# Optimization experiments

Measured on AMD Instinct MI355X. Metric: run time of the kernel, lower is better.

Reference implementation:

```python
import jax, jax.numpy as jnp
import numpy as np

L, H, E, T, B, V = 8, 16, 1024, 1024, 2, 800
D = E // H  # head_size = 64
STD = 0.02


def setup_inputs() -> dict:
    key = jax.random.key(0)
    ks = iter(jax.random.split(key, 32))

    def nrm(shape):
        return jax.random.normal(next(ks), shape, jnp.float32) * STD

    latlong = jax.random.uniform(next(ks), (B, T, 2), jnp.float32)
    wl = jax.random.uniform(next(ks), (B, T, 1), jnp.float32, minval=3.0, maxval=11.0)
    inp = {
        "idx": jnp.concatenate([latlong, wl], axis=-1),  # [B,T,3]
        "tok_table": nrm((V, E)),
        "pos_W": nrm((2, E)),
        "pos_b": jnp.zeros((E,), jnp.float32),
        # stacked per-layer params (per-head q/k/v linears fused into [E,E])
        "Wq": nrm((L, E, E)),
        "Wk": nrm((L, E, E)),
        "Wv": nrm((L, E, E)),
        "Wo": nrm((L, E, E)),
        "bo": jnp.zeros((L, E), jnp.float32),
        "W1": nrm((L, E, 4 * E)),
        "b1": jnp.zeros((L, 4 * E), jnp.float32),
        "W2": nrm((L, 4 * E, E)),
        "b2": jnp.zeros((L, E), jnp.float32),
        "ln1_g": jnp.ones((L, E), jnp.float32),
        "ln1_b": jnp.zeros((L, E), jnp.float32),
        "ln2_g": jnp.ones((L, E), jnp.float32),
        "ln2_b": jnp.zeros((L, E), jnp.float32),
        "lnf_g": jnp.ones((E,), jnp.float32),
        "lnf_b": jnp.zeros((E,), jnp.float32),
        "lm_W": nrm((E, V)),
        "lm_b": jnp.zeros((V,), jnp.float32),
    }
    return inp


def _ln(x, g, b, eps=1e-5):
    m = x.mean(-1, keepdims=True)
    v = x.var(-1, keepdims=True)
    return (x - m) * jax.lax.rsqrt(v + eps) * g + b


def _block(x, p):
    Wq, Wk, Wv, Wo, bo, W1, b1, W2, b2, g1, be1, g2, be2 = p
    Bx, Tx, _ = x.shape
    h = _ln(x, g1, be1)
    q = (h @ Wq).reshape(Bx, Tx, H, D)
    k = (h @ Wk).reshape(Bx, Tx, H, D)
    v = (h @ Wv).reshape(Bx, Tx, H, D)
    scores = jnp.einsum('bqhd,bkhd->bhqk', q, k) * (D ** -0.5)
    mask = jnp.tril(jnp.ones((Tx, Tx), bool))  # causal
    scores = jnp.where(mask, scores, -jnp.inf)
    w = jax.nn.softmax(scores, axis=-1)  # dropout=0 (eval) -> identity
    attn = jnp.einsum('bhqk,bkhd->bqhd', w, v).reshape(Bx, Tx, E)
    x = x + attn @ Wo + bo
    h = _ln(x, g2, be2)
    x = x + jax.nn.relu(h @ W1 + b1) @ W2 + b2
    return x


def reference(idx, tok_table, pos_W, pos_b, Wq, Wk, Wv, Wo, bo, W1, b1, W2, b2,
              ln1_g, ln1_b, ln2_g, ln2_b, lnf_g, lnf_b, lm_W, lm_b):
    # water level channel -> token id in [0, V-1]
    idx_wl = jnp.clip(jnp.round(idx[..., 2] * 100.0 - 300.0), 0, V - 1).astype(jnp.int32)
    tok_emb = tok_table[idx_wl]                      # [B,T,E]
    pos_emb = idx[..., :2] @ pos_W + pos_b           # [B,T,E]
    x = tok_emb + pos_emb

    params = (Wq, Wk, Wv, Wo, bo, W1, b1, W2, b2, ln1_g, ln1_b, ln2_g, ln2_b)

    def body(carry, p):
        return _block(carry, p), None

    x, _ = jax.lax.scan(body, x, params)
    x = _ln(x, lnf_g, lnf_b)
    logits = x @ lm_W + lm_b                         # [B,T,V]
    return logits
```

## Files before the change

kernel.cpp:

```cpp
#include <hip/hip_runtime.h>
#include <hip/hip_bf16.h>

#define L_ 8
#define H_ 16
#define E_ 1024
#define T_ 1024
#define B_ 2
#define V_ 800
#define D_ 64
#define FF_ 4096
#define N_ (B_ * T_)
#define QS_ 3072

typedef unsigned short u16;
typedef __bf16 bf16x8 __attribute__((ext_vector_type(8)));
typedef float f32x4 __attribute__((ext_vector_type(4)));

__device__ __forceinline__ u16 f2b(float f) {
    unsigned int u = __float_as_uint(f);
    unsigned int r = (u + 0x7fffu + ((u >> 16) & 1u)) >> 16;
    return (u16)r;
}

__device__ __forceinline__ void gld16(const u16* g, u16* l) {
    __builtin_amdgcn_global_load_lds(
        (__attribute__((address_space(1))) void*)(uintptr_t)g,
        (__attribute__((address_space(3))) void*)(unsigned)(uintptr_t)l,
        16, 0, 0);
}

__global__ __launch_bounds__(256) void embed_k(
    const float* __restrict__ idx, const float* __restrict__ tok,
    const float* __restrict__ posW, const float* __restrict__ posb,
    float* __restrict__ x)
{
    int row = blockIdx.x;
    int e = threadIdx.x * 4;
    float lat = idx[row * 3 + 0];
    float lon = idx[row * 3 + 1];
    float wl  = idx[row * 3 + 2];
    float tf = rintf(wl * 100.0f - 300.0f);
    tf = fminf(fmaxf(tf, 0.0f), (float)(V_ - 1));
    int tkn = (int)tf;

    float4 tv = *(const float4*)(tok + (size_t)tkn * E_ + e);
    float4 p0 = *(const float4*)(posW + e);
    float4 p1 = *(const float4*)(posW + E_ + e);
    float4 pb = *(const float4*)(posb + e);
    float4 ov;
    ov.x = tv.x + lat * p0.x + lon * p1.x + pb.x;
    ov.y = tv.y + lat * p0.y + lon * p1.y + pb.y;
    ov.z = tv.z + lat * p0.z + lon * p1.z + pb.z;
    ov.w = tv.w + lat * p0.w + lon * p1.w + pb.w;
    *(float4*)(x + (size_t)row * E_ + e) = ov;
}

__global__ __launch_bounds__(256) void ln_k(
    const float* __restrict__ x, const float* __restrict__ g,
    const float* __restrict__ bta, u16* __restrict__ out)
{
    __shared__ float rs[4], rq[4];
    int row = blockIdx.x;
    int tid = threadIdx.x;
    const float* xr = x + (size_t)row * E_;
    float4 xv = *(const float4*)(xr + tid * 4);
    float s = xv.x + xv.y + xv.z + xv.w;
    float q = xv.x * xv.x + xv.y * xv.y + xv.z * xv.z + xv.w * xv.w;
    #pragma unroll
    for (int off = 32; off; off >>= 1) {
        s += __shfl_xor(s, off, 64);
        q += __shfl_xor(q, off, 64);
    }
    int wv = tid >> 6, ln = tid & 63;
    if (ln == 0) { rs[wv] = s; rq[wv] = q; }
    __syncthreads();
    s = rs[0] + rs[1] + rs[2] + rs[3];
    q = rq[0] + rq[1] + rq[2] + rq[3];
    float mean = s * (1.0f / E_);
    float var  = q * (1.0f / E_) - mean * mean;
    float inv  = 1.0f / sqrtf(var + 1e-5f);
    int c = tid * 4;
    float4 gv = *(const float4*)(g + c);
    float4 bv = *(const float4*)(bta + c);
    ushort4 ov;
    ov.x = f2b((xv.x - mean) * inv * gv.x + bv.x);
    ov.y = f2b((xv.y - mean) * inv * gv.y + bv.y);
    ov.z = f2b((xv.z - mean) * inv * gv.z + bv.z);
    ov.w = f2b((xv.w - mean) * inv * gv.w + bv.w);
    *(ushort4*)(out + (size_t)row * E_ + c) = ov;
}

__global__ __launch_bounds__(256) void comb_ln_k(
    const float* __restrict__ Cp, const float* __restrict__ bias,
    float* __restrict__ x, const float* __restrict__ g,
    const float* __restrict__ bta, u16* __restrict__ hout)
{
    __shared__ float rs[4], rq[4];
    int row = blockIdx.x;
    int tid = threadIdx.x;
    int c = tid * 4;
    size_t off = (size_t)row * E_ + c;
    const size_t total = (size_t)N_ * E_;
    float4 p0 = *(const float4*)(Cp + off);
    float4 p1 = *(const float4*)(Cp + total + off);
    float4 xv = *(const float4*)(x + off);
    float4 bv = *(const float4*)(bias + c);
    xv.x += p0.x + p1.x + bv.x;
    xv.y += p0.y + p1.y + bv.y;
    xv.z += p0.z + p1.z + bv.z;
    xv.w += p0.w + p1.w + bv.w;
    *(float4*)(x + off) = xv;

    float s = xv.x + xv.y + xv.z + xv.w;
    float q = xv.x * xv.x + xv.y * xv.y + xv.z * xv.z + xv.w * xv.w;
    #pragma unroll
    for (int o = 32; o; o >>= 1) {
        s += __shfl_xor(s, o, 64);
        q += __shfl_xor(q, o, 64);
    }
    int wv = tid >> 6, ln = tid & 63;
    if (ln == 0) { rs[wv] = s; rq[wv] = q; }
    __syncthreads();
    s = rs[0] + rs[1] + rs[2] + rs[3];
    q = rq[0] + rq[1] + rq[2] + rq[3];
    float mean = s * (1.0f / E_);
    float var  = q * (1.0f / E_) - mean * mean;
    float inv  = 1.0f / sqrtf(var + 1e-5f);
    float4 gv = *(const float4*)(g + c);
    float4 bb = *(const float4*)(bta + c);
    ushort4 ov;
    ov.x = f2b((xv.x - mean) * inv * gv.x + bb.x);
    ov.y = f2b((xv.y - mean) * inv * gv.y + bb.y);
    ov.z = f2b((xv.z - mean) * inv * gv.z + bb.z);
    ov.w = f2b((xv.w - mean) * inv * gv.w + bb.w);
    *(ushort4*)(hout + off) = ov;
}

__device__ __forceinline__ void wtrans_body(
    const float* __restrict__ W, u16* __restrict__ Wt, int K, int M,
    int m0, int k0)
{
    __shared__ float tile[64][65];
    int tid = threadIdx.x;
    int rr = tid >> 4, c4 = (tid & 15) * 4;
    if (m0 + 64 <= M) {
        #pragma unroll
        for (int p = 0; p < 4; p++) {
            int kk = rr + p * 16;
            float4 v4 = *(const float4*)(W + (size_t)(k0 + kk) * M + m0 + c4);
            tile[kk][c4 + 0] = v4.x; tile[kk][c4 + 1] = v4.y;
            tile[kk][c4 + 2] = v4.z; tile[kk][c4 + 3] = v4.w;
        }
    } else {
        #pragma unroll
        for (int p = 0; p < 4; p++) {
            int kk = rr + p * 16;
            const float* wr = W + (size_t)(k0 + kk) * M;
            #pragma unroll
            for (int c = 0; c < 4; c++) {
                int m = m0 + c4 + c;
                tile[kk][c4 + c] = (m < M) ? wr[m] : 0.0f;
            }
        }
    }
    __syncthreads();
    #pragma unroll
    for (int p = 0; p < 4; p++) {
        int ml = rr + p * 16;
        ushort4 o;
        o.x = f2b(tile[c4 + 0][ml]);
        o.y = f2b(tile[c4 + 1][ml]);
        o.z = f2b(tile[c4 + 2][ml]);
        o.w = f2b(tile[c4 + 3][ml]);
        *(ushort4*)(Wt + (size_t)(m0 + ml) * K + k0 + c4) = o;
    }
}

__global__ __launch_bounds__(256) void wtrans_k(
    const float* __restrict__ W, u16* __restrict__ Wt, int K, int M)
{
    wtrans_body(W, Wt, K, M, blockIdx.x * 64, blockIdx.y * 64);
}

__global__ __launch_bounds__(256) void wtrans_all_k(
    const float* __restrict__ Wq, const float* __restrict__ Wk,
    const float* __restrict__ Wv, const float* __restrict__ Wo,
    const float* __restrict__ W1, const float* __restrict__ W2,
    u16* __restrict__ wqkv_t, u16* __restrict__ wo_t,
    u16* __restrict__ w1_t, u16* __restrict__ w2_t)
{
    int bx = blockIdx.x, by = blockIdx.y, z = blockIdx.z;
    const size_t M1 = 1024 * 1024;
    if (z < 4) {
        if (bx >= 16) return;
        const float* W = (z == 0) ? Wq : (z == 1) ? Wk : (z == 2) ? Wv : Wo;
        u16* dst = (z < 3) ? (wqkv_t + (size_t)z * M1) : wo_t;
        wtrans_body(W, dst, E_, E_, bx * 64, by * 64);
    } else if (z == 4) {
        wtrans_body(W1, w1_t, E_, FF_, bx * 64, by * 64);
    } else {
        int id = by * 64 + bx;
        int mb = id >> 6, kb = id & 63;
        wtrans_body(W2, w2_t, FF_, E_, mb * 64, kb * 64);
    }
}

__global__ __launch_bounds__(256) void gemm_bf16(
    const u16* __restrict__ A, const u16* __restrict__ Bt,
    const float* __restrict__ bias, const float* __restrict__ res,
    float* __restrict__ Cf, u16* __restrict__ Cb, float* __restrict__ Cp,
    int K, int M, int relu)
{
    __shared__ __align__(16) u16 As[128 * 32];
    __shared__ __align__(16) u16 Bs[128 * 32];
    int tid = threadIdx.x;
    int bm = blockIdx.y * 128, bn = blockIdx.x * 128;
    int zz = blockIdx.z;
    int kslice = K / (int)gridDim.z;
    int lane = tid & 63, wv = tid >> 6;
    int l15 = lane & 15, q4 = lane >> 4;
    int wm = (wv & 1) * 64, wn = (wv >> 1) * 64;

    const u16* ga = A + (size_t)(bm + (tid >> 2)) * K + zz * kslice + (tid & 3) * 8;
    const u16* gb = Bt + (size_t)(bn + (tid >> 2)) * K + zz * kslice + (tid & 3) * 8;
    size_t gstep = (size_t)64 * K;
    u16* lA0 = As + wv * (16 * 32);
    u16* lB0 = Bs + wv * (16 * 32);

    f32x4 acc[4][4];
    #pragma unroll
    for (int i = 0; i < 4; i++)
        #pragma unroll
        for (int j = 0; j < 4; j++)
            acc[i][j] = (f32x4){0.0f, 0.0f, 0.0f, 0.0f};

    for (int k0 = 0; k0 < kslice; k0 += 32) {
        gld16(ga, lA0);
        gld16(ga + gstep, lA0 + 64 * 32);
        gld16(gb, lB0);
        gld16(gb + gstep, lB0 + 64 * 32);
        ga += 32; gb += 32;
        __syncthreads();

        const bf16x8* Ap = (const bf16x8*)As + (wm + l15) * 4 + q4;
        const bf16x8* Bp = (const bf16x8*)Bs + (wn + l15) * 4 + q4;
        bf16x8 af[4], bg[4];
        #pragma unroll
        for (int i = 0; i < 4; i++) { af[i] = Ap[i * 64]; bg[i] = Bp[i * 64]; }
        #pragma unroll
        for (int i = 0; i < 4; i++)
            #pragma unroll
            for (int j = 0; j < 4; j++)
                acc[i][j] = __builtin_amdgcn_mfma_f32_16x16x32_bf16(
                    af[i], bg[j], acc[i][j], 0, 0, 0);
        __syncthreads();
    }

    size_t poff = (size_t)zz * N_ * M;
    #pragma unroll
    for (int i = 0; i < 4; i++) {
        int r0 = bm + wm + i * 16 + q4 * 4;
        #pragma unroll
        for (int j = 0; j < 4; j++) {
            int col = bn + wn + j * 16 + l15;
            if (col < M) {
                if (Cp) {
                    #pragma unroll
                    for (int r = 0; r < 4; r++)
                        Cp[poff + (size_t)(r0 + r) * M + col] = acc[i][j][r];
                } else {
                    float bv = bias ? bias[col] : 0.0f;
                    #pragma unroll
                    for (int r = 0; r < 4; r++) {
                        size_t off = (size_t)(r0 + r) * M + col;
                        float v = acc[i][j][r] + bv;
                        if (res) v += res[off];
                        if (relu) v = fmaxf(v, 0.0f);
                        if (Cb) Cb[off] = f2b(v); else Cf[off] = v;
                    }
                }
            }
        }
    }
}

__global__ __launch_bounds__(256) void combine_k(
    const float* __restrict__ Cp, const float* __restrict__ bias,
    float* __restrict__ Cf, int M, int total)
{
    int e = (blockIdx.x * 256 + threadIdx.x) * 4;
    if (e >= total) return;
    float4 a = *(const float4*)(Cp + e);
    float4 b = *(const float4*)(Cp + (size_t)total + e);
    a.x += b.x; a.y += b.y; a.z += b.z; a.w += b.w;
    int col = e % M;
    if (bias) {
        float4 bv = *(const float4*)(bias + col);
        a.x += bv.x; a.y += bv.y; a.z += bv.z; a.w += bv.w;
    }
    *(float4*)(Cf + e) = a;
}

__global__ __launch_bounds__(256) void vtrans_k(
    const u16* __restrict__ QKV, u16* __restrict__ Vt)
{
    __shared__ u16 tile[64][72];
    int t0 = blockIdx.x * 64, h = blockIdx.y, b = blockIdx.z;
    int tid = threadIdx.x;
    int row = tid >> 3, c8 = (tid & 7) * 8;
    #pragma unroll
    for (int p = 0; p < 2; p++) {
        int t = row + p * 32;
        *(float4*)&tile[t][c8] = *(const float4*)(
            QKV + (size_t)(b * T_ + t0 + t) * QS_ + 2 * E_ + h * D_ + c8);
    }
    __syncthreads();
    #pragma unroll
    for (int p = 0; p < 2; p++) {
        int d = row + p * 32;
        u16 o[8];
        #pragma unroll
        for (int j = 0; j < 8; j++) o[j] = tile[c8 + j][d];
        *(ushort4*)(Vt + ((size_t)(b * H_ + h) * D_ + d) * T_ + t0 + c8) =
            *(ushort4*)&o[0];
        *(ushort4*)(Vt + ((size_t)(b * H_ + h) * D_ + d) * T_ + t0 + c8 + 4) =
            *(ushort4*)&o[4];
    }
}

__global__ __launch_bounds__(256) void attn_mfma_k(
    const u16* __restrict__ QKV, const u16* __restrict__ Vt,
    u16* __restrict__ O)
{
    __shared__ __align__(16) u16 Ps[4][16 * 72];
    int tid = threadIdx.x;
    int wv = tid >> 6, lane = tid & 63;
    int c = lane & 15, q4 = lane >> 4;
    int qb = (int)(gridDim.x - 1) - (int)blockIdx.x;
    int h = blockIdx.y, b = blockIdx.z;
    int q0 = qb * 64 + wv * 16;
    const float scale = 0.125f;

    const u16* qrow = QKV + (size_t)(b * T_ + q0 + c) * QS_ + h * D_;
    bf16x8 qf0 = *(const bf16x8*)(qrow + q4 * 8);
    bf16x8 qf1 = *(const bf16x8*)(qrow + 32 + q4 * 8);

    const u16* kbase  = QKV + (size_t)b * T_ * QS_ + E_ + h * D_;
    const u16* vtbase = Vt + (size_t)(b * H_ + h) * D_ * T_;

    float l_acc[4] = {0.0f, 0.0f, 0.0f, 0.0f};
    f32x4 acc_o[4];
    #pragma unroll
    for (int nt = 0; nt < 4; nt++) acc_o[nt] = (f32x4){0.f, 0.f, 0.f, 0.f};

    u16* ps = &Ps[wv][0];

    for (int kt = 0; kt <= qb; kt++) {
        int k0 = kt * 64;
        bool diag = (kt == qb);

        bf16x8 kf[4][2];
        #pragma unroll
        for (int j = 0; j < 4; j++) {
            const u16* kr = kbase + (size_t)(k0 + 16 * j + c) * QS_ + q4 * 8;
            kf[j][0] = *(const bf16x8*)(kr);
            kf[j][1] = *(const bf16x8*)(kr + 32);
        }

        #pragma unroll
        for (int j = 0; j < 4; j++) {
            f32x4 sa = (f32x4){0.f, 0.f, 0.f, 0.f};
            sa = __builtin_amdgcn_mfma_f32_16x16x32_bf16(qf0, kf[j][0], sa, 0, 0, 0);
            sa = __builtin_amdgcn_mfma_f32_16x16x32_bf16(qf1, kf[j][1], sa, 0, 0, 0);
            #pragma unroll
            for (int r = 0; r < 4; r++) {
                bool masked = diag && (k0 + 16 * j + c > q0 + 4 * q4 + r);
                float pj = masked ? 0.0f : __expf(sa[r] * scale);
                l_acc[r] += pj;
                ps[(4 * q4 + r) * 72 + 16 * j + c] = f2b(pj);
            }
        }
        bf16x8 pf0 = *(const bf16x8*)(ps + c * 72 + q4 * 8);
        bf16x8 pf1 = *(const bf16x8*)(ps + c * 72 + 32 + q4 * 8);

        bf16x8 vf[4][2];
        #pragma unroll
        for (int nt = 0; nt < 4; nt++) {
            const u16* vr = vtbase + (size_t)(16 * nt + c) * T_ + k0 + q4 * 8;
            vf[nt][0] = *(const bf16x8*)(vr);
            vf[nt][1] = *(const bf16x8*)(vr + 32);
        }

        #pragma unroll
        for (int nt = 0; nt < 4; nt++) {
            acc_o[nt] = __builtin_amdgcn_mfma_f32_16x16x32_bf16(pf0, vf[nt][0], acc_o[nt], 0, 0, 0);
            acc_o[nt] = __builtin_amdgcn_mfma_f32_16x16x32_bf16(pf1, vf[nt][1], acc_o[nt], 0, 0, 0);
        }
    }

    #pragma unroll
    for (int r = 0; r < 4; r++) {
        float ts = l_acc[r];
        ts += __shfl_xor(ts, 1, 64);
        ts += __shfl_xor(ts, 2, 64);
        ts += __shfl_xor(ts, 4, 64);
        ts += __shfl_xor(ts, 8, 64);
        l_acc[r] = ts;
    }

    #pragma unroll
    for (int r = 0; r < 4; r++) {
        float inv = 1.0f / l_acc[r];
        size_t orow = (size_t)(b * T_ + q0 + 4 * q4 + r) * E_ + h * D_;
        #pragma unroll
        for (int nt = 0; nt < 4; nt++)
            O[orow + 16 * nt + c] = f2b(acc_o[nt][r] * inv);
    }
}

extern "C" void kernel_launch(void* const* d_in, const int* in_sizes, int n_in,
                              void* d_out, int out_size, void* d_ws, size_t ws_size,
                              hipStream_t stream)
{
    const float* idx   = (const float*)d_in[0];
    const float* tok   = (const float*)d_in[1];
    const float* posW  = (const float*)d_in[2];
    const float* posb  = (const float*)d_in[3];
    const float* Wq    = (const float*)d_in[4];
    const float* Wk    = (const float*)d_in[5];
    const float* Wv    = (const float*)d_in[6];
    const float* Wo    = (const float*)d_in[7];
    const float* bo    = (const float*)d_in[8];
    const float* W1    = (const float*)d_in[9];
    const float* b1    = (const float*)d_in[10];
    const float* W2    = (const float*)d_in[11];
    const float* b2    = (const float*)d_in[12];
    const float* ln1g  = (const float*)d_in[13];
    const float* ln1b  = (const float*)d_in[14];
    const float* ln2g  = (const float*)d_in[15];
    const float* ln2b  = (const float*)d_in[16];
    const float* lnfg  = (const float*)d_in[17];
    const float* lnfb  = (const float*)d_in[18];
    const float* lmW   = (const float*)d_in[19];
    const float* lmb   = (const float*)d_in[20];
    float* out = (float*)d_out;

    const size_t M1 = 1024 * 1024;
    float* ws    = (float*)d_ws;
    float* x     = ws;
    float* cpart = x + 2 * M1;
    u16* qkv   = (u16*)(cpart + 4 * M1);
    u16* vt    = qkv + 6 * M1;
    u16* h_bf  = vt + 2 * M1;
    u16* ao_bf = h_bf + 2 * M1;
    u16* ff_bf = ao_bf + 2 * M1;
    u16* wq_t  = ff_bf + 8 * M1;
    u16* wo_t  = wq_t + 3 * M1;
    u16* w1_t  = wo_t + 1 * M1;
    u16* w2_t  = w1_t + 4 * M1;
    u16* wlm_t = w2_t + 4 * M1;

    dim3 blk(256);
    dim3 gQKV(3072 / 128, N_ / 128, 1);
    dim3 gWo(1024 / 128, N_ / 128, 2);
    dim3 gW1(4096 / 128, N_ / 128, 1);
    dim3 gW2(1024 / 128, N_ / 128, 2);
    dim3 gLM(7, N_ / 128, 2);
    dim3 gAT(T_ / 64, H_, B_);
    dim3 gWT(64, 16, 6);
    dim3 tLM(14, 16);
    int totLM = N_ * V_;
    dim3 cLM(totLM / 4 / 256);

    embed_k<<<N_, blk, 0, stream>>>(idx, tok, posW, posb, x);
    ln_k<<<N_, blk, 0, stream>>>(x, ln1g, ln1b, h_bf);

    for (int l = 0; l < L_; l++) {
        size_t oEE = (size_t)l * E_ * E_;
        size_t oE  = (size_t)l * E_;
        size_t oEF = (size_t)l * E_ * FF_;
        size_t oF  = (size_t)l * FF_;

        wtrans_all_k<<<gWT, blk, 0, stream>>>(
            Wq + oEE, Wk + oEE, Wv + oEE, Wo + oEE, W1 + oEF, W2 + oEF,
            wq_t, wo_t, w1_t, w2_t);
        gemm_bf16<<<gQKV, blk, 0, stream>>>(h_bf, wq_t, nullptr, nullptr,
                                            nullptr, qkv, nullptr, E_, QS_, 0);
        vtrans_k<<<gAT, blk, 0, stream>>>(qkv, vt);
        attn_mfma_k<<<gAT, blk, 0, stream>>>(qkv, vt, ao_bf);
        gemm_bf16<<<gWo, blk, 0, stream>>>(ao_bf, wo_t, nullptr, nullptr,
                                           nullptr, nullptr, cpart, E_, E_, 0);
        comb_ln_k<<<N_, blk, 0, stream>>>(cpart, bo + oE, x,
                                          ln2g + oE, ln2b + oE, h_bf);
        gemm_bf16<<<gW1, blk, 0, stream>>>(h_bf, w1_t, b1 + oF, nullptr,
                                           nullptr, ff_bf, nullptr, E_, FF_, 1);
        gemm_bf16<<<gW2, blk, 0, stream>>>(ff_bf, w2_t, nullptr, nullptr,
                                           nullptr, nullptr, cpart, FF_, E_, 0);
        if (l < L_ - 1) {
            comb_ln_k<<<N_, blk, 0, stream>>>(cpart, b2 + oE, x,
                                              ln1g + oE + E_, ln1b + oE + E_, h_bf);
        } else {
            comb_ln_k<<<N_, blk, 0, stream>>>(cpart, b2 + oE, x,
                                              lnfg, lnfb, h_bf);
        }
    }

    wtrans_k<<<tLM, blk, 0, stream>>>(lmW, wlm_t, E_, V_);
    gemm_bf16<<<gLM, blk, 0, stream>>>(h_bf, wlm_t, nullptr, nullptr,
                                       nullptr, nullptr, cpart, E_, V_, 0);
    combine_k<<<cLM, blk, 0, stream>>>(cpart, lmb, out, V_, totLM);
}
```

Before: 2.174 ms.

## Triple-buffer GEMM loads, raise split-K to four, fuse V transpose into QKV epilogue

```diff
diff --git a/kernel.cpp b/kernel.cpp
--- a/kernel.cpp
+++ b/kernel.cpp
@@ -103,12 +103,14 @@
     const size_t total = (size_t)N_ * E_;
     float4 p0 = *(const float4*)(Cp + off);
     float4 p1 = *(const float4*)(Cp + total + off);
+    float4 p2 = *(const float4*)(Cp + 2 * total + off);
+    float4 p3 = *(const float4*)(Cp + 3 * total + off);
     float4 xv = *(const float4*)(x + off);
     float4 bv = *(const float4*)(bias + c);
-    xv.x += p0.x + p1.x + bv.x;
-    xv.y += p0.y + p1.y + bv.y;
-    xv.z += p0.z + p1.z + bv.z;
-    xv.w += p0.w + p1.w + bv.w;
+    xv.x += p0.x + p1.x + p2.x + p3.x + bv.x;
+    xv.y += p0.y + p1.y + p2.y + p3.y + bv.y;
+    xv.z += p0.z + p1.z + p2.z + p3.z + bv.z;
+    xv.w += p0.w + p1.w + p2.w + p3.w + bv.w;
     *(float4*)(x + off) = xv;
 
     float s = xv.x + xv.y + xv.z + xv.w;
@@ -209,10 +211,10 @@
     const u16* __restrict__ A, const u16* __restrict__ Bt,
     const float* __restrict__ bias, const float* __restrict__ res,
     float* __restrict__ Cf, u16* __restrict__ Cb, float* __restrict__ Cp,
-    int K, int M, int relu)
-{
-    __shared__ __align__(16) u16 As[128 * 32];
-    __shared__ __align__(16) u16 Bs[128 * 32];
+    u16* __restrict__ VtOut, int K, int M, int relu)
+{
+    __shared__ __align__(16) u16 As[3][128 * 32];
+    __shared__ __align__(16) u16 Bs[3][128 * 32];
     int tid = threadIdx.x;
     int bm = blockIdx.y * 128, bn = blockIdx.x * 128;
     int zz = blockIdx.z;
@@ -224,8 +226,7 @@
     const u16* ga = A + (size_t)(bm + (tid >> 2)) * K + zz * kslice + (tid & 3) * 8;
     const u16* gb = Bt + (size_t)(bn + (tid >> 2)) * K + zz * kslice + (tid & 3) * 8;
     size_t gstep = (size_t)64 * K;
-    u16* lA0 = As + wv * (16 * 32);
-    u16* lB0 = Bs + wv * (16 * 32);
+    int lofs = wv * (16 * 32);
 
     f32x4 acc[4][4];
     #pragma unroll
@@ -234,16 +235,31 @@
         for (int j = 0; j < 4; j++)
             acc[i][j] = (f32x4){0.0f, 0.0f, 0.0f, 0.0f};
 
-    for (int k0 = 0; k0 < kslice; k0 += 32) {
-        gld16(ga, lA0);
-        gld16(ga + gstep, lA0 + 64 * 32);
-        gld16(gb, lB0);
-        gld16(gb + gstep, lB0 + 64 * 32);
-        ga += 32; gb += 32;
-        __syncthreads();
-
-        const bf16x8* Ap = (const bf16x8*)As + (wm + l15) * 4 + q4;
-        const bf16x8* Bp = (const bf16x8*)Bs + (wn + l15) * 4 + q4;
+    auto STAGE = [&](int buf, int t) {
+        const u16* a0 = ga + t * 32;
+        const u16* b0 = gb + t * 32;
+        u16* la = &As[buf][0] + lofs;
+        u16* lb = &Bs[buf][0] + lofs;
+        gld16(a0, la);
+        gld16(a0 + gstep, la + 64 * 32);
+        gld16(b0, lb);
+        gld16(b0 + gstep, lb + 64 * 32);
+    };
+
+    int nt = kslice / 32;
+    STAGE(0, 0);
+    if (nt > 1) STAGE(1, 1);
+
+    for (int t = 0; t < nt; ++t) {
+        if (t + 1 < nt)
+            asm volatile("s_waitcnt vmcnt(4) lgkmcnt(0)\n\ts_barrier" ::: "memory");
+        else
+            asm volatile("s_waitcnt vmcnt(0) lgkmcnt(0)\n\ts_barrier" ::: "memory");
+        if (t + 2 < nt) STAGE((t + 2) % 3, t + 2);
+
+        int cur = t % 3;
+        const bf16x8* Ap = (const bf16x8*)(&As[cur][0]) + (wm + l15) * 4 + q4;
+        const bf16x8* Bp = (const bf16x8*)(&Bs[cur][0]) + (wn + l15) * 4 + q4;
         bf16x8 af[4], bg[4];
         #pragma unroll
         for (int i = 0; i < 4; i++) { af[i] = Ap[i * 64]; bg[i] = Bp[i * 64]; }
@@ -253,7 +269,6 @@
             for (int j = 0; j < 4; j++)
                 acc[i][j] = __builtin_amdgcn_mfma_f32_16x16x32_bf16(
                     af[i], bg[j], acc[i][j], 0, 0, 0);
-        __syncthreads();
     }
 
     size_t poff = (size_t)zz * N_ * M;
@@ -270,13 +285,24 @@
                         Cp[poff + (size_t)(r0 + r) * M + col] = acc[i][j][r];
                 } else {
                     float bv = bias ? bias[col] : 0.0f;
+                    u16 vb[4];
                     #pragma unroll
                     for (int r = 0; r < 4; r++) {
                         size_t off = (size_t)(r0 + r) * M + col;
                         float v = acc[i][j][r] + bv;
                         if (res) v += res[off];
                         if (relu) v = fmaxf(v, 0.0f);
-                        if (Cb) Cb[off] = f2b(v); else Cf[off] = v;
+                        u16 hv = f2b(v);
+                        vb[r] = hv;
+                        if (Cb) Cb[off] = hv; else Cf[off] = v;
+                    }
+                    if (VtOut && col >= 2 * E_) {
+                        int vcol = col - 2 * E_;
+                        int hh = vcol >> 6, dd = vcol & 63;
+                        int bb = r0 >> 10, t0 = r0 & 1023;
+                        *(ushort4*)(VtOut +
+                            ((size_t)(bb * H_ + hh) * D_ + dd) * T_ + t0) =
+                            *(ushort4*)vb;
                     }
                 }
             }
@@ -299,33 +325,6 @@
         a.x += bv.x; a.y += bv.y; a.z += bv.z; a.w += bv.w;
     }
     *(float4*)(Cf + e) = a;
-}
-
-__global__ __launch_bounds__(256) void vtrans_k(
-    const u16* __restrict__ QKV, u16* __restrict__ Vt)
-{
-    __shared__ u16 tile[64][72];
-    int t0 = blockIdx.x * 64, h = blockIdx.y, b = blockIdx.z;
-    int tid = threadIdx.x;
-    int row = tid >> 3, c8 = (tid & 7) * 8;
-    #pragma unroll
-    for (int p = 0; p < 2; p++) {
-        int t = row + p * 32;
-        *(float4*)&tile[t][c8] = *(const float4*)(
-            QKV + (size_t)(b * T_ + t0 + t) * QS_ + 2 * E_ + h * D_ + c8);
-    }
-    __syncthreads();
-    #pragma unroll
-    for (int p = 0; p < 2; p++) {
-        int d = row + p * 32;
-        u16 o[8];
-        #pragma unroll
-        for (int j = 0; j < 8; j++) o[j] = tile[c8 + j][d];
-        *(ushort4*)(Vt + ((size_t)(b * H_ + h) * D_ + d) * T_ + t0 + c8) =
-            *(ushort4*)&o[0];
-        *(ushort4*)(Vt + ((size_t)(b * H_ + h) * D_ + d) * T_ + t0 + c8 + 4) =
-            *(ushort4*)&o[4];
-    }
 }
 
 __global__ __launch_bounds__(256) void attn_mfma_k(
@@ -449,7 +448,7 @@
     float* ws    = (float*)d_ws;
     float* x     = ws;
     float* cpart = x + 2 * M1;
-    u16* qkv   = (u16*)(cpart + 4 * M1);
+    u16* qkv   = (u16*)(cpart + 8 * M1);
     u16* vt    = qkv + 6 * M1;
     u16* h_bf  = vt + 2 * M1;
     u16* ao_bf = h_bf + 2 * M1;
@@ -462,9 +461,9 @@
 
     dim3 blk(256);
     dim3 gQKV(3072 / 128, N_ / 128, 1);
-    dim3 gWo(1024 / 128, N_ / 128, 2);
+    dim3 gWo(1024 / 128, N_ / 128, 4);
     dim3 gW1(4096 / 128, N_ / 128, 1);
-    dim3 gW2(1024 / 128, N_ / 128, 2);
+    dim3 gW2(1024 / 128, N_ / 128, 4);
     dim3 gLM(7, N_ / 128, 2);
     dim3 gAT(T_ / 64, H_, B_);
     dim3 gWT(64, 16, 6);
@@ -485,17 +484,16 @@
             Wq + oEE, Wk + oEE, Wv + oEE, Wo + oEE, W1 + oEF, W2 + oEF,
             wq_t, wo_t, w1_t, w2_t);
         gemm_bf16<<<gQKV, blk, 0, stream>>>(h_bf, wq_t, nullptr, nullptr,
-                                            nullptr, qkv, nullptr, E_, QS_, 0);
-        vtrans_k<<<gAT, blk, 0, stream>>>(qkv, vt);
+                                            nullptr, qkv, nullptr, vt, E_, QS_, 0);
         attn_mfma_k<<<gAT, blk, 0, stream>>>(qkv, vt, ao_bf);
         gemm_bf16<<<gWo, blk, 0, stream>>>(ao_bf, wo_t, nullptr, nullptr,
-                                           nullptr, nullptr, cpart, E_, E_, 0);
+                                           nullptr, nullptr, cpart, nullptr, E_, E_, 0);
         comb_ln_k<<<N_, blk, 0, stream>>>(cpart, bo + oE, x,
                                           ln2g + oE, ln2b + oE, h_bf);
         gemm_bf16<<<gW1, blk, 0, stream>>>(h_bf, w1_t, b1 + oF, nullptr,
-                                           nullptr, ff_bf, nullptr, E_, FF_, 1);
+                                           nullptr, ff_bf, nullptr, nullptr, E_, FF_, 1);
         gemm_bf16<<<gW2, blk, 0, stream>>>(ff_bf, w2_t, nullptr, nullptr,
-                                           nullptr, nullptr, cpart, FF_, E_, 0);
+                                           nullptr, nullptr, cpart, nullptr, FF_, E_, 0);
         if (l < L_ - 1) {
             comb_ln_k<<<N_, blk, 0, stream>>>(cpart, b2 + oE, x,
                                               ln1g + oE + E_, ln1b + oE + E_, h_bf);
@@ -507,6 +505,6 @@
 
     wtrans_k<<<tLM, blk, 0, stream>>>(lmW, wlm_t, E_, V_);
     gemm_bf16<<<gLM, blk, 0, stream>>>(h_bf, wlm_t, nullptr, nullptr,
-                                       nullptr, nullptr, cpart, E_, V_, 0);
+                                       nullptr, nullptr, cpart, nullptr, E_, V_, 0);
     combine_k<<<cLM, blk, 0, stream>>>(cpart, lmb, out, V_, totLM);
 }
```

New measurement: 1.858 ms. 1.17x faster.
